# Performance work log

Hardware: AMD Instinct MI355X
Metric: run time of the kernel (lower is better)

## Reference

```python
import jax, jax.numpy as jnp
import numpy as np

B, T, C = 2, 1024, 2048
E, TOPK = 8, 2
F_MOE = 1408
F_SHARED = 5632


def setup_inputs() -> dict:
    key = jax.random.key(0)
    ks = jax.random.split(key, 9)
    s = 0.02
    return {
        "x": jax.random.normal(ks[0], (B, T, C), dtype=jnp.float32),
        "gate_w": jax.random.normal(ks[1], (E, C), dtype=jnp.float32) * s,
        "expert_fc1": jax.random.normal(ks[2], (E, F_MOE, C), dtype=jnp.float32) * s,
        "expert_fc2": jax.random.normal(ks[3], (E, F_MOE, C), dtype=jnp.float32) * s,
        "expert_proj": jax.random.normal(ks[4], (E, C, F_MOE), dtype=jnp.float32) * s,
        "shared_fc1": jax.random.normal(ks[5], (F_SHARED, C), dtype=jnp.float32) * s,
        "shared_fc2": jax.random.normal(ks[6], (F_SHARED, C), dtype=jnp.float32) * s,
        "shared_proj": jax.random.normal(ks[7], (C, F_SHARED), dtype=jnp.float32) * s,
        "shared_gate_w": jax.random.normal(ks[8], (1, C), dtype=jnp.float32) * s,
    }


def reference(x, gate_w, expert_fc1, expert_fc2, expert_proj,
              shared_fc1, shared_fc2, shared_proj, shared_gate_w):
    b, t, c = x.shape
    xf = x.reshape(-1, c)                                   # [N, C]
    n = xf.shape[0]

    # router: softmax in fp32, then top-k
    router = xf @ gate_w.T                                  # [N, E]
    probs = jax.nn.softmax(router.astype(jnp.float32), axis=1).astype(x.dtype)
    top_p, top_i = jax.lax.top_k(probs, TOPK)               # [N, k]

    # dense combine weights: prob where selected else 0 (top-k indices are distinct)
    combine = jnp.zeros((n, E), dtype=x.dtype).at[
        jnp.arange(n)[:, None], top_i].set(top_p)            # [N, E]

    # per-expert SwiGLU MLP, computed densely then weighted by combine
    h1 = jnp.einsum('nc,efc->enf', xf, expert_fc1)          # [E, N, F]
    h2 = jnp.einsum('nc,efc->enf', xf, expert_fc2)
    h = jax.nn.silu(h1) * h2
    out_e = jnp.einsum('enf,ecf->enc', h, expert_proj)      # [E, N, C]
    y = jnp.einsum('ne,enc->nc', combine, out_e)            # [N, C]

    # shared expert with sigmoid gate
    s1 = xf @ shared_fc1.T
    s2 = xf @ shared_fc2.T
    shared = (jax.nn.silu(s1) * s2) @ shared_proj.T         # [N, C]
    y = y + jax.nn.sigmoid(xf @ shared_gate_w.T) * shared
    return y.reshape(b, t, c)
```

## Files before the change

### kernel.cpp

```cpp
#include <hip/hip_runtime.h>
#include <hip/hip_bf16.h>
#include <math.h>
#include <stdint.h>

#define N_TOK   2048
#define C_DIM   2048
#define E_NUM   8
#define F_MOE   1408
#define F_SH    5632
#define SLOTS   4096
#define PADROWS 4608

typedef __bf16 bf16;
typedef __bf16 bf16x8 __attribute__((ext_vector_type(8)));
typedef __bf16 bf16x4 __attribute__((ext_vector_type(4)));
typedef float  f32x4  __attribute__((ext_vector_type(4)));

__device__ __forceinline__ f32x4 mfma16(bf16x8 a, bf16x8 b, f32x4 c) {
    return __builtin_amdgcn_mfma_f32_16x16x32_bf16(a, b, c, 0, 0, 0);
}
__device__ __forceinline__ void gload16(const void* g, void* l) {
    __builtin_amdgcn_global_load_lds(
        (const __attribute__((address_space(1))) void*)g,
        (__attribute__((address_space(3))) void*)l, 16, 0, 0);
}
#define RAWBAR() asm volatile("s_barrier" ::: "memory")
#define VMCNT8() asm volatile("s_waitcnt vmcnt(8)" ::: "memory")
#define VMCNT4() asm volatile("s_waitcnt vmcnt(4)" ::: "memory")
#define VMCNT0() asm volatile("s_waitcnt vmcnt(0)" ::: "memory")

__global__ void router_kernel(const float* __restrict__ x,
                              const float* __restrict__ gate_w,
                              const float* __restrict__ sgate_w,
                              int* __restrict__ slotexp,
                              float* __restrict__ slotp,
                              float* __restrict__ sig)
{
    const int n   = blockIdx.x;
    const int tid = threadIdx.x;
    const float* xr = x + (size_t)n * C_DIM;
    const int c0 = tid * 8;

    float xv[8];
#pragma unroll
    for (int j = 0; j < 8; ++j) xv[j] = xr[c0 + j];

    float dots[9];
#pragma unroll
    for (int e = 0; e < 9; ++e) {
        const float* wr = (e < 8) ? (gate_w + (size_t)e * C_DIM) : sgate_w;
        float p = 0.f;
#pragma unroll
        for (int j = 0; j < 8; ++j) p += xv[j] * wr[c0 + j];
#pragma unroll
        for (int off = 32; off > 0; off >>= 1) p += __shfl_down(p, off);
        dots[e] = p;
    }

    __shared__ float red[4][9];
    const int wid = tid >> 6, lane = tid & 63;
    if (lane == 0) {
#pragma unroll
        for (int e = 0; e < 9; ++e) red[wid][e] = dots[e];
    }
    __syncthreads();
    if (tid == 0) {
        float l[9];
#pragma unroll
        for (int e = 0; e < 9; ++e)
            l[e] = red[0][e] + red[1][e] + red[2][e] + red[3][e];
        float mx = l[0];
#pragma unroll
        for (int e = 1; e < 8; ++e) mx = fmaxf(mx, l[e]);
        float p[8], s = 0.f;
#pragma unroll
        for (int e = 0; e < 8; ++e) { p[e] = expf(l[e] - mx); s += p[e]; }
        const float inv = 1.f / s;
#pragma unroll
        for (int e = 0; e < 8; ++e) p[e] *= inv;
        int i1 = 0;
#pragma unroll
        for (int e = 1; e < 8; ++e) if (p[e] > p[i1]) i1 = e;
        int i2 = (i1 == 0) ? 1 : 0;
#pragma unroll
        for (int e = 0; e < 8; ++e) if (e != i1 && p[e] > p[i2]) i2 = e;
        slotexp[2 * n]     = i1;  slotp[2 * n]     = p[i1];
        slotexp[2 * n + 1] = i2;  slotp[2 * n + 1] = p[i2];
        sig[n] = 1.f / (1.f + expf(-l[8]));
    }
}

__global__ void scatter_kernel(const int* __restrict__ slotexp,
                               int* __restrict__ counts, int* __restrict__ bases,
                               int* __restrict__ pos_of, int* __restrict__ row_token)
{
    const int tid = threadIdx.x;
    const int w = tid >> 6, lane = tid & 63;
    __shared__ int cnt[E_NUM], base[E_NUM];

    int run = 0;
    for (int s0 = 0; s0 < SLOTS; s0 += 64) {
        int e = slotexp[s0 + lane];
        unsigned long long m = __ballot(e == w);
        run += __popcll(m);
    }
    if (lane == 0) cnt[w] = run;
    __syncthreads();
    if (tid == 0) {
        int b = 0;
        for (int e = 0; e < E_NUM; ++e) { base[e] = b; b += cnt[e]; }
    }
    __syncthreads();
    run = 0;
    for (int s0 = 0; s0 < SLOTS; s0 += 64) {
        const int s = s0 + lane;
        const int e = slotexp[s];
        unsigned long long m = __ballot(e == w);
        if (e == w) {
            const unsigned long long lt = (lane == 0) ? 0ull : (~0ull >> (64 - lane));
            const int pos = base[w] + run + __popcll(m & lt);
            pos_of[s]      = pos;
            row_token[pos] = s >> 1;
        }
        run += __popcll(m);
    }
    if (lane == 0) { counts[w] = cnt[w]; bases[w] = base[w]; }
}

struct CvtArgs {
    const float* in[7];
    bf16*        out[7];
    int          cum[8];
};

__global__ void cvt_all_kernel(CvtArgs a)
{
    int b = blockIdx.x;
    int s = 0;
#pragma unroll
    for (int k = 1; k < 7; ++k) s += (b >= a.cum[k]);
    const size_t base = (size_t)(b - a.cum[s]) * 8192;
    const float* in = a.in[s];
    bf16* out = a.out[s];
    const int t4 = threadIdx.x * 4;
    f32x4 v[8];
#pragma unroll
    for (int c = 0; c < 8; ++c)
        v[c] = *(const f32x4*)(in + base + c * 1024 + t4);
#pragma unroll
    for (int c = 0; c < 8; ++c) {
        bf16x4 o;
#pragma unroll
        for (int j = 0; j < 4; ++j) o[j] = (bf16)v[c][j];
        *(bf16x4*)(out + base + c * 1024 + t4) = o;
    }
}

__global__ void gather_kernel(const bf16* __restrict__ Xs,
                              const int* __restrict__ row_token,
                              bf16* __restrict__ Xg)
{
    const int pos = blockIdx.x;
    const int t   = row_token[pos];
    const bf16x8* s = (const bf16x8*)(Xs + (size_t)t * C_DIM);
    bf16x8*       d = (bf16x8*)(Xg + (size_t)pos * C_DIM);
    d[threadIdx.x] = s[threadIdx.x];
}

template<bool DUAL, int KSPLIT>
__device__ __forceinline__ void gemm_body(
    const bf16* __restrict__ A, int lda,
    const bf16* __restrict__ B1g, const bf16* __restrict__ B2g, size_t strideB,
    bf16* __restrict__ OUTh, bf16* __restrict__ OUTq, int ldo, size_t strideOut,
    int base, int cnt, int e, int yt, int nt, int kp, int K, char* lds)
{
    const int KT = (K / 64) / KSPLIT;
    const int H  = 2 * KT;

    const int m0 = base + yt * 256;
    const int tid = threadIdx.x;
    const int w = tid >> 6, lane = tid & 63;

    const int l3  = lane >> 3;
    const int chS = (lane & 7) ^ l3;
    const int hiS = chS >> 2, ccS = chS & 3;
    const int rl  = w * 16 + 2 * l3 + hiS;
    const size_t lda2 = (size_t)lda * 2, K2 = (size_t)K * 2;
    const size_t kpoff = (size_t)kp * KT * 128;

    const char* aSrc0 = (const char*)A + (size_t)(m0 + rl)       * lda2 + ccS * 16 + kpoff;
    const char* aSrc1 = (const char*)A + (size_t)(m0 + 128 + rl) * lda2 + ccS * 16 + kpoff;
    const bf16* B1 = B1g + (size_t)e * strideB;
    const char* bSrc0;
    const char* bSrc1;
    if constexpr (DUAL) {
        const bf16* B2 = B2g + (size_t)e * strideB;
        bSrc0 = (const char*)B1 + (size_t)(nt * 128 + rl) * K2 + ccS * 16 + kpoff;
        bSrc1 = (const char*)B2 + (size_t)(nt * 128 + rl) * K2 + ccS * 16 + kpoff;
    } else {
        bSrc0 = (const char*)B1 + (size_t)(nt * 256 + rl)       * K2 + ccS * 16 + kpoff;
        bSrc1 = (const char*)B1 + (size_t)(nt * 256 + 128 + rl) * K2 + ccS * 16 + kpoff;
    }
    char* ldsw = lds + w * 1024;

    auto issue = [&](int h) {
        const size_t ko = (size_t)(h >> 1) * 128 + (size_t)(h & 1) * 64;
        char* d = ldsw + (h & 3) * 32768;
        gload16(aSrc0 + ko, d);
        gload16(aSrc1 + ko, d + 8192);
        gload16(bSrc0 + ko, d + 16384);
        gload16(bSrc1 + ko, d + 24576);
    };

    const int wm = w >> 2, wn = w & 3;
    const int fr = lane & 15, fq = lane >> 4;
    const int chRd = (((fr & 1) << 2) | fq) ^ ((fr >> 1) & 7);
    uint32_t aOff[8], bOff[4];
#pragma unroll
    for (int m = 0; m < 8; ++m)
        aOff[m] = (uint32_t)((wm * 64 + m * 8 + (fr >> 1)) * 128 + chRd * 16);
#pragma unroll
    for (int n = 0; n < 4; ++n) {
        int rp;
        if constexpr (DUAL)
            rp = (n < 2) ? (wn * 16 + n * 8) : (64 + wn * 16 + (n - 2) * 8);
        else
            rp = wn * 32 + n * 8;
        rp += (fr >> 1);
        bOff[n] = (uint32_t)(16384 + rp * 128 + chRd * 16);
    }

    f32x4 acc[8][4] = {};

    auto compute_half = [&](int h) {
        const char* LB = lds + (h & 3) * 32768;
        bf16x8 af[4], bf[4];
#pragma unroll
        for (int n = 0; n < 4; ++n) bf[n] = *(const bf16x8*)(LB + bOff[n]);
#pragma unroll
        for (int m = 0; m < 4; ++m) af[m] = *(const bf16x8*)(LB + aOff[m]);
        RAWBAR(); __builtin_amdgcn_sched_barrier(0);
        __builtin_amdgcn_s_setprio(1);
#pragma unroll
        for (int m = 0; m < 4; ++m)
#pragma unroll
            for (int n = 0; n < 4; ++n)
                acc[m][n] = mfma16(af[m], bf[n], acc[m][n]);
        __builtin_amdgcn_s_setprio(0);
#pragma unroll
        for (int m = 0; m < 4; ++m) af[m] = *(const bf16x8*)(LB + aOff[4 + m]);
        RAWBAR(); __builtin_amdgcn_sched_barrier(0);
        __builtin_amdgcn_s_setprio(1);
#pragma unroll
        for (int m = 0; m < 4; ++m)
#pragma unroll
            for (int n = 0; n < 4; ++n)
                acc[4 + m][n] = mfma16(af[m], bf[n], acc[4 + m][n]);
        __builtin_amdgcn_s_setprio(0);
    };

    issue(0); issue(1); issue(2);

    for (int h = 0; h < H - 3; ++h) {
        VMCNT8();
        RAWBAR();
        issue(h + 3);
        compute_half(h);
    }
    VMCNT8(); RAWBAR(); compute_half(H - 3);
    VMCNT4(); RAWBAR(); compute_half(H - 2);
    VMCNT0(); RAWBAR(); compute_half(H - 1);

    const int rb0 = m0 + wm * 128;
    const int rend = base + cnt;
#pragma unroll
    for (int m = 0; m < 8; ++m) {
#pragma unroll
        for (int j = 0; j < 4; ++j) {
            const int grow = rb0 + m * 16 + fq * 4 + j;
            if (grow >= rend) continue;
            if constexpr (DUAL) {
#pragma unroll
                for (int n = 0; n < 2; ++n) {
                    const int gcol = nt * 128 + wn * 32 + n * 16 + fr;
                    const float h1 = acc[m][n][j];
                    const float h2 = acc[m][n + 2][j];
                    OUTh[(size_t)grow * ldo + gcol] =
                        (bf16)(h1 / (1.f + expf(-h1)) * h2);
                }
            } else {
                bf16* O = OUTq + (size_t)kp * strideOut;
#pragma unroll
                for (int n = 0; n < 4; ++n) {
                    const int gcol = nt * 256 + wn * 64 + n * 16 + fr;
                    O[(size_t)grow * ldo + gcol] = (bf16)acc[m][n][j];
                }
            }
        }
    }
}

template<bool DUAL, bool GROUPED, int KSPLIT>
__global__ __launch_bounds__(512, 1)
void gemm8(const bf16* __restrict__ A, int lda,
           const bf16* __restrict__ B1g, const bf16* __restrict__ B2g,
           size_t strideB,
           bf16* __restrict__ OUTh, bf16* __restrict__ OUTq, int ldo,
           size_t strideOut,
           const int* __restrict__ bases, const int* __restrict__ counts,
           int K)
{
    __shared__ char lds[131072];
    int e, yt, nt, kp, base, cnt;
    if constexpr (GROUPED) {
        e = blockIdx.x; yt = blockIdx.y; nt = blockIdx.z; kp = 0;
        base = bases[e]; cnt = counts[e];
        if (yt * 256 >= cnt) return;
    } else {
        nt = blockIdx.x; yt = blockIdx.y; kp = (KSPLIT > 1) ? blockIdx.z : 0;
        e = 0; base = 0; cnt = N_TOK;
    }
    gemm_body<DUAL, KSPLIT>(A, lda, B1g, B2g, strideB, OUTh, OUTq, ldo,
                            strideOut, base, cnt, e, yt, nt, kp, K, lds);
}

#define FC0_TILES 352

__global__ __launch_bounds__(512, 1)
void gemm_fc(const bf16* __restrict__ Xs, const bf16* __restrict__ Xg,
             const bf16* __restrict__ Wsfc1, const bf16* __restrict__ Wsfc2,
             const bf16* __restrict__ Wefc1, const bf16* __restrict__ Wefc2,
             bf16* __restrict__ Hs, bf16* __restrict__ Hm,
             const int* __restrict__ bases, const int* __restrict__ counts)
{
    __shared__ char lds[131072];
    const int id = blockIdx.x;
    if (id < FC0_TILES) {
        const int nt = id % 44, yt = id / 44;
        gemm_body<true, 1>(Xs, C_DIM, Wsfc1, Wsfc2, 0, Hs, nullptr, F_SH, 0,
                           0, N_TOK, 0, yt, nt, 0, C_DIM, lds);
    } else {
        const int lid = id - FC0_TILES;
        const int e = lid & 7, yt = (lid >> 3) & 15, nt = lid >> 7;
        const int base = bases[e], cnt = counts[e];
        if (yt * 256 >= cnt) return;
        gemm_body<true, 1>(Xg, C_DIM, Wefc1, Wefc2, (size_t)F_MOE * C_DIM,
                           Hm, nullptr, F_MOE, 0,
                           base, cnt, e, yt, nt, 0, C_DIM, lds);
    }
}

__global__ void combine_kernel(const bf16* __restrict__ SP,
                               const bf16* __restrict__ EP,
                               const int* __restrict__ pos_of,
                               const float* __restrict__ slotp,
                               const float* __restrict__ sig,
                               float* __restrict__ y)
{
    const int n  = blockIdx.x;
    const int p0 = pos_of[2 * n], p1 = pos_of[2 * n + 1];
    const float w0 = slotp[2 * n], w1 = slotp[2 * n + 1], sg = sig[n];
    const size_t PS = (size_t)N_TOK * C_DIM;
    const size_t cidx = (size_t)n * C_DIM + threadIdx.x * 8;

    bf16x8 s0 = *(const bf16x8*)(SP + cidx);
    bf16x8 s1 = *(const bf16x8*)(SP + cidx + PS);
    bf16x8 s2 = *(const bf16x8*)(SP + cidx + 2 * PS);
    bf16x8 s3 = *(const bf16x8*)(SP + cidx + 3 * PS);
    bf16x8 a0 = *(const bf16x8*)(EP + (size_t)p0 * C_DIM + threadIdx.x * 8);
    bf16x8 a1 = *(const bf16x8*)(EP + (size_t)p1 * C_DIM + threadIdx.x * 8);

    float out[8];
#pragma unroll
    for (int j = 0; j < 8; ++j) {
        const float ssum = (float)s0[j] + (float)s1[j] + (float)s2[j] + (float)s3[j];
        out[j] = sg * ssum + w0 * (float)a0[j] + w1 * (float)a1[j];
    }
    f32x4 o0, o1;
#pragma unroll
    for (int j = 0; j < 4; ++j) { o0[j] = out[j]; o1[j] = out[4 + j]; }
    *(f32x4*)(y + cidx)     = o0;
    *(f32x4*)(y + cidx + 4) = o1;
}

extern "C" void kernel_launch(void* const* d_in, const int* in_sizes, int n_in,
                              void* d_out, int out_size, void* d_ws, size_t ws_size,
                              hipStream_t stream)
{
    const float* x     = (const float*)d_in[0];
    const float* gatew = (const float*)d_in[1];
    const float* efc1  = (const float*)d_in[2];
    const float* efc2  = (const float*)d_in[3];
    const float* eproj = (const float*)d_in[4];
    const float* sfc1  = (const float*)d_in[5];
    const float* sfc2  = (const float*)d_in[6];
    const float* sproj = (const float*)d_in[7];
    const float* sgate = (const float*)d_in[8];
    float* y = (float*)d_out;

    char* w = (char*)d_ws;
    size_t off = 0;
    auto take = [&](size_t bytes) {
        char* p = w + off;
        off = (off + bytes + 255) & ~(size_t)255;
        return p;
    };
    int*   counts    = (int*)  take(E_NUM * 4);
    int*   bases     = (int*)  take(E_NUM * 4);
    int*   slotexp   = (int*)  take(SLOTS * 4);
    float* slotp     = (float*)take(SLOTS * 4);
    int*   pos_of    = (int*)  take(SLOTS * 4);
    int*   row_token = (int*)  take(PADROWS * 4);
    float* sig       = (float*)take(N_TOK * 4);
    bf16*  Xs        = (bf16*) take((size_t)N_TOK   * C_DIM * 2);
    bf16*  Xg        = (bf16*) take((size_t)PADROWS * C_DIM * 2);
    bf16*  Hs        = (bf16*) take((size_t)N_TOK   * F_SH  * 2);
    bf16*  Hm        = (bf16*) take((size_t)PADROWS * F_MOE * 2);
    bf16*  SP        = (bf16*) take((size_t)4 * N_TOK * C_DIM * 2);
    bf16*  EP        = (bf16*) take((size_t)PADROWS * C_DIM * 2);
    bf16*  Wefc1     = (bf16*) take((size_t)E_NUM * F_MOE * C_DIM * 2);
    bf16*  Wefc2     = (bf16*) take((size_t)E_NUM * F_MOE * C_DIM * 2);
    bf16*  Weproj    = (bf16*) take((size_t)E_NUM * C_DIM * F_MOE * 2);
    bf16*  Wsfc1     = (bf16*) take((size_t)F_SH * C_DIM * 2);
    bf16*  Wsfc2     = (bf16*) take((size_t)F_SH * C_DIM * 2);
    bf16*  Wsproj    = (bf16*) take((size_t)C_DIM * F_SH * 2);
    (void)ws_size; (void)in_sizes; (void)n_in; (void)out_size;

    CvtArgs ca;
    const int nbx  = (N_TOK * C_DIM) / 8192;
    const int nbe  = (E_NUM * F_MOE * C_DIM) / 8192;
    const int nbs  = (F_SH * C_DIM) / 8192;
    ca.in[0] = x;     ca.out[0] = Xs;
    ca.in[1] = efc1;  ca.out[1] = Wefc1;
    ca.in[2] = efc2;  ca.out[2] = Wefc2;
    ca.in[3] = eproj; ca.out[3] = Weproj;
    ca.in[4] = sfc1;  ca.out[4] = Wsfc1;
    ca.in[5] = sfc2;  ca.out[5] = Wsfc2;
    ca.in[6] = sproj; ca.out[6] = Wsproj;
    ca.cum[0] = 0;
    ca.cum[1] = nbx;
    ca.cum[2] = nbx + nbe;
    ca.cum[3] = nbx + 2 * nbe;
    ca.cum[4] = nbx + 3 * nbe;
    ca.cum[5] = nbx + 3 * nbe + nbs;
    ca.cum[6] = nbx + 3 * nbe + 2 * nbs;
    ca.cum[7] = nbx + 3 * nbe + 3 * nbs;
    cvt_all_kernel<<<ca.cum[7], 256, 0, stream>>>(ca);

    router_kernel<<<N_TOK, 256, 0, stream>>>(x, gatew, sgate, slotexp, slotp, sig);
    scatter_kernel<<<1, 512, 0, stream>>>(slotexp, counts, bases, pos_of, row_token);
    gather_kernel<<<SLOTS, 256, 0, stream>>>(Xs, row_token, Xg);

    gemm_fc<<<FC0_TILES + E_NUM * (SLOTS / 256) * (F_MOE / 128), 512, 0, stream>>>(
        Xs, Xg, Wsfc1, Wsfc2, Wefc1, Wefc2, Hs, Hm, bases, counts);

    gemm8<false, false, 4><<<dim3(C_DIM / 256, N_TOK / 256, 4), 512, 0, stream>>>(
        Hs, F_SH, Wsproj, nullptr, 0, nullptr, SP, C_DIM, (size_t)N_TOK * C_DIM,
        nullptr, nullptr, F_SH);

    gemm8<false, true, 1><<<dim3(E_NUM, SLOTS / 256, C_DIM / 256), 512, 0, stream>>>(
        Hm, F_MOE, Weproj, nullptr, (size_t)C_DIM * F_MOE, nullptr, EP, C_DIM, 0,
        bases, counts, F_MOE);

    combine_kernel<<<N_TOK, 256, 0, stream>>>(SP, EP, pos_of, slotp, sig, y);
}
```

Measured before the change: 448.1 us.

## Fuse fp32-to-bf16 weight conversion into GEMM B-tile loading

Drops the standalone pass that converted all expert and shared weights to bf16. The GEMMs now read fp32 weights directly into registers, convert them, and write bf16 into LDS, while the A operand keeps the async global-to-LDS path. The pipeline is rebuilt with two register buffers, adjusted vmcnt waits and an lgkm wait before each barrier. This removes a full read-and-write of every weight, but doubles the weight bytes each GEMM tile fetches and, since tiles re-read weights, repeats the conversion work. The extra VGPR pressure and VALU conversion sit in the inner loop.

Measured after the change: 473.1 us. +5.6%, slower.

```diff
diff --git a/kernel.cpp b/kernel.cpp
--- a/kernel.cpp
+++ b/kernel.cpp
@@ -26,8 +26,10 @@
 }
 #define RAWBAR() asm volatile("s_barrier" ::: "memory")
 #define VMCNT8() asm volatile("s_waitcnt vmcnt(8)" ::: "memory")
-#define VMCNT4() asm volatile("s_waitcnt vmcnt(4)" ::: "memory")
+#define VMCNT6() asm volatile("s_waitcnt vmcnt(6)" ::: "memory")
 #define VMCNT0() asm volatile("s_waitcnt vmcnt(0)" ::: "memory")
+#define LGKM0()  asm volatile("s_waitcnt lgkmcnt(0)" ::: "memory")
+#define CFENCE() asm volatile("" ::: "memory")
 
 __global__ void router_kernel(const float* __restrict__ x,
                               const float* __restrict__ gate_w,
@@ -127,21 +129,9 @@
     if (lane == 0) { counts[w] = cnt[w]; bases[w] = base[w]; }
 }
 
-struct CvtArgs {
-    const float* in[7];
-    bf16*        out[7];
-    int          cum[8];
-};
-
-__global__ void cvt_all_kernel(CvtArgs a)
-{
-    int b = blockIdx.x;
-    int s = 0;
-#pragma unroll
-    for (int k = 1; k < 7; ++k) s += (b >= a.cum[k]);
-    const size_t base = (size_t)(b - a.cum[s]) * 8192;
-    const float* in = a.in[s];
-    bf16* out = a.out[s];
+__global__ void cvt_x_kernel(const float* __restrict__ in, bf16* __restrict__ out)
+{
+    const size_t base = (size_t)blockIdx.x * 8192;
     const int t4 = threadIdx.x * 4;
     f32x4 v[8];
 #pragma unroll
@@ -170,7 +160,7 @@
 template<bool DUAL, int KSPLIT>
 __device__ __forceinline__ void gemm_body(
     const bf16* __restrict__ A, int lda,
-    const bf16* __restrict__ B1g, const bf16* __restrict__ B2g, size_t strideB,
+    const float* __restrict__ B1g, const float* __restrict__ B2g, size_t strideB,
     bf16* __restrict__ OUTh, bf16* __restrict__ OUTq, int ldo, size_t strideOut,
     int base, int cnt, int e, int yt, int nt, int kp, int K, char* lds)
 {
@@ -185,31 +175,49 @@
     const int chS = (lane & 7) ^ l3;
     const int hiS = chS >> 2, ccS = chS & 3;
     const int rl  = w * 16 + 2 * l3 + hiS;
-    const size_t lda2 = (size_t)lda * 2, K2 = (size_t)K * 2;
-    const size_t kpoff = (size_t)kp * KT * 128;
-
-    const char* aSrc0 = (const char*)A + (size_t)(m0 + rl)       * lda2 + ccS * 16 + kpoff;
-    const char* aSrc1 = (const char*)A + (size_t)(m0 + 128 + rl) * lda2 + ccS * 16 + kpoff;
-    const bf16* B1 = B1g + (size_t)e * strideB;
-    const char* bSrc0;
-    const char* bSrc1;
+    const size_t lda2 = (size_t)lda * 2;
+    const size_t K4 = (size_t)K * 4;
+    const size_t kpoffA = (size_t)kp * KT * 128;
+    const size_t kpoffB = (size_t)kp * KT * 256;
+
+    const char* aSrc0 = (const char*)A + (size_t)(m0 + rl)       * lda2 + ccS * 16 + kpoffA;
+    const char* aSrc1 = (const char*)A + (size_t)(m0 + 128 + rl) * lda2 + ccS * 16 + kpoffA;
+    const float* B1 = B1g + (size_t)e * strideB;
+    const char* bSrc0f;
+    const char* bSrc1f;
     if constexpr (DUAL) {
-        const bf16* B2 = B2g + (size_t)e * strideB;
-        bSrc0 = (const char*)B1 + (size_t)(nt * 128 + rl) * K2 + ccS * 16 + kpoff;
-        bSrc1 = (const char*)B2 + (size_t)(nt * 128 + rl) * K2 + ccS * 16 + kpoff;
+        const float* B2 = B2g + (size_t)e * strideB;
+        bSrc0f = (const char*)B1 + (size_t)(nt * 128 + rl) * K4 + ccS * 32 + kpoffB;
+        bSrc1f = (const char*)B2 + (size_t)(nt * 128 + rl) * K4 + ccS * 32 + kpoffB;
     } else {
-        bSrc0 = (const char*)B1 + (size_t)(nt * 256 + rl)       * K2 + ccS * 16 + kpoff;
-        bSrc1 = (const char*)B1 + (size_t)(nt * 256 + 128 + rl) * K2 + ccS * 16 + kpoff;
+        bSrc0f = (const char*)B1 + (size_t)(nt * 256 + rl)       * K4 + ccS * 32 + kpoffB;
+        bSrc1f = (const char*)B1 + (size_t)(nt * 256 + 128 + rl) * K4 + ccS * 32 + kpoffB;
     }
     char* ldsw = lds + w * 1024;
 
-    auto issue = [&](int h) {
+    auto issueA = [&](int h) {
         const size_t ko = (size_t)(h >> 1) * 128 + (size_t)(h & 1) * 64;
         char* d = ldsw + (h & 3) * 32768;
         gload16(aSrc0 + ko, d);
         gload16(aSrc1 + ko, d + 8192);
-        gload16(bSrc0 + ko, d + 16384);
-        gload16(bSrc1 + ko, d + 24576);
+    };
+    auto issueB = [&](int h, f32x4 (&set)[4]) {
+        const size_t ko = (size_t)(h >> 1) * 256 + (size_t)(h & 1) * 128;
+        set[0] = *(const f32x4*)(bSrc0f + ko);
+        set[1] = *(const f32x4*)(bSrc0f + ko + 16);
+        set[2] = *(const f32x4*)(bSrc1f + ko);
+        set[3] = *(const f32x4*)(bSrc1f + ko + 16);
+    };
+    auto writeB = [&](int h, f32x4 (&set)[4]) {
+        bf16x8 w0, w1;
+#pragma unroll
+        for (int j = 0; j < 4; ++j) {
+            w0[j] = (bf16)set[0][j]; w0[4 + j] = (bf16)set[1][j];
+            w1[j] = (bf16)set[2][j]; w1[4 + j] = (bf16)set[3][j];
+        }
+        char* bd = ldsw + (h & 3) * 32768 + 16384 + lane * 16;
+        *(bf16x8*)bd = w0;
+        *(bf16x8*)(bd + 8192) = w1;
     };
 
     const int wm = w >> 2, wn = w & 3;
@@ -259,17 +267,30 @@
         __builtin_amdgcn_s_setprio(0);
     };
 
-    issue(0); issue(1); issue(2);
-
-    for (int h = 0; h < H - 3; ++h) {
-        VMCNT8();
+    f32x4 bsA[4], bsB[4];
+
+    auto ITER = [&](int h, f32x4 (&set)[4], int wc) {
+        if (wc == 8) { VMCNT8(); } else if (wc == 6) { VMCNT6(); } else { VMCNT0(); }
+        writeB(h, set);
+        LGKM0();
         RAWBAR();
-        issue(h + 3);
+        if (h + 2 < H) { issueB(h + 2, set); } CFENCE();
+        if (h + 3 < H) { issueA(h + 3); }    CFENCE();
         compute_half(h);
-    }
-    VMCNT8(); RAWBAR(); compute_half(H - 3);
-    VMCNT4(); RAWBAR(); compute_half(H - 2);
-    VMCNT0(); RAWBAR(); compute_half(H - 1);
+    };
+
+    issueA(0); CFENCE();
+    issueB(0, bsA); CFENCE();
+    issueA(1); CFENCE();
+    issueB(1, bsB); CFENCE();
+    issueA(2); CFENCE();
+
+    for (int h = 0; h < H - 2; h += 2) {
+        ITER(h, bsA, 8);
+        ITER(h + 1, bsB, 8);
+    }
+    ITER(H - 2, bsA, 6);
+    ITER(H - 1, bsB, 0);
 
     const int rb0 = m0 + wm * 128;
     const int rend = base + cnt;
@@ -303,7 +324,7 @@
 template<bool DUAL, bool GROUPED, int KSPLIT>
 __global__ __launch_bounds__(512, 1)
 void gemm8(const bf16* __restrict__ A, int lda,
-           const bf16* __restrict__ B1g, const bf16* __restrict__ B2g,
+           const float* __restrict__ B1g, const float* __restrict__ B2g,
            size_t strideB,
            bf16* __restrict__ OUTh, bf16* __restrict__ OUTq, int ldo,
            size_t strideOut,
@@ -328,8 +349,8 @@
 
 __global__ __launch_bounds__(512, 1)
 void gemm_fc(const bf16* __restrict__ Xs, const bf16* __restrict__ Xg,
-             const bf16* __restrict__ Wsfc1, const bf16* __restrict__ Wsfc2,
-             const bf16* __restrict__ Wefc1, const bf16* __restrict__ Wefc2,
+             const float* __restrict__ sfc1, const float* __restrict__ sfc2,
+             const float* __restrict__ efc1, const float* __restrict__ efc2,
              bf16* __restrict__ Hs, bf16* __restrict__ Hm,
              const int* __restrict__ bases, const int* __restrict__ counts)
 {
@@ -337,14 +358,14 @@
     const int id = blockIdx.x;
     if (id < FC0_TILES) {
         const int nt = id % 44, yt = id / 44;
-        gemm_body<true, 1>(Xs, C_DIM, Wsfc1, Wsfc2, 0, Hs, nullptr, F_SH, 0,
+        gemm_body<true, 1>(Xs, C_DIM, sfc1, sfc2, 0, Hs, nullptr, F_SH, 0,
                            0, N_TOK, 0, yt, nt, 0, C_DIM, lds);
     } else {
         const int lid = id - FC0_TILES;
         const int e = lid & 7, yt = (lid >> 3) & 15, nt = lid >> 7;
         const int base = bases[e], cnt = counts[e];
         if (yt * 256 >= cnt) return;
-        gemm_body<true, 1>(Xg, C_DIM, Wefc1, Wefc2, (size_t)F_MOE * C_DIM,
+        gemm_body<true, 1>(Xg, C_DIM, efc1, efc2, (size_t)F_MOE * C_DIM,
                            Hm, nullptr, F_MOE, 0,
                            base, cnt, e, yt, nt, 0, C_DIM, lds);
     }
@@ -418,48 +439,23 @@
     bf16*  Hm        = (bf16*) take((size_t)PADROWS * F_MOE * 2);
     bf16*  SP        = (bf16*) take((size_t)4 * N_TOK * C_DIM * 2);
     bf16*  EP        = (bf16*) take((size_t)PADROWS * C_DIM * 2);
-    bf16*  Wefc1     = (bf16*) take((size_t)E_NUM * F_MOE * C_DIM * 2);
-    bf16*  Wefc2     = (bf16*) take((size_t)E_NUM * F_MOE * C_DIM * 2);
-    bf16*  Weproj    = (bf16*) take((size_t)E_NUM * C_DIM * F_MOE * 2);
-    bf16*  Wsfc1     = (bf16*) take((size_t)F_SH * C_DIM * 2);
-    bf16*  Wsfc2     = (bf16*) take((size_t)F_SH * C_DIM * 2);
-    bf16*  Wsproj    = (bf16*) take((size_t)C_DIM * F_SH * 2);
     (void)ws_size; (void)in_sizes; (void)n_in; (void)out_size;
 
-    CvtArgs ca;
-    const int nbx  = (N_TOK * C_DIM) / 8192;
-    const int nbe  = (E_NUM * F_MOE * C_DIM) / 8192;
-    const int nbs  = (F_SH * C_DIM) / 8192;
-    ca.in[0] = x;     ca.out[0] = Xs;
-    ca.in[1] = efc1;  ca.out[1] = Wefc1;
-    ca.in[2] = efc2;  ca.out[2] = Wefc2;
-    ca.in[3] = eproj; ca.out[3] = Weproj;
-    ca.in[4] = sfc1;  ca.out[4] = Wsfc1;
-    ca.in[5] = sfc2;  ca.out[5] = Wsfc2;
-    ca.in[6] = sproj; ca.out[6] = Wsproj;
-    ca.cum[0] = 0;
-    ca.cum[1] = nbx;
-    ca.cum[2] = nbx + nbe;
-    ca.cum[3] = nbx + 2 * nbe;
-    ca.cum[4] = nbx + 3 * nbe;
-    ca.cum[5] = nbx + 3 * nbe + nbs;
-    ca.cum[6] = nbx + 3 * nbe + 2 * nbs;
-    ca.cum[7] = nbx + 3 * nbe + 3 * nbs;
-    cvt_all_kernel<<<ca.cum[7], 256, 0, stream>>>(ca);
+    cvt_x_kernel<<<(N_TOK * C_DIM) / 8192, 256, 0, stream>>>(x, Xs);
 
     router_kernel<<<N_TOK, 256, 0, stream>>>(x, gatew, sgate, slotexp, slotp, sig);
     scatter_kernel<<<1, 512, 0, stream>>>(slotexp, counts, bases, pos_of, row_token);
     gather_kernel<<<SLOTS, 256, 0, stream>>>(Xs, row_token, Xg);
 
     gemm_fc<<<FC0_TILES + E_NUM * (SLOTS / 256) * (F_MOE / 128), 512, 0, stream>>>(
-        Xs, Xg, Wsfc1, Wsfc2, Wefc1, Wefc2, Hs, Hm, bases, counts);
+        Xs, Xg, sfc1, sfc2, efc1, efc2, Hs, Hm, bases, counts);
 
     gemm8<false, false, 4><<<dim3(C_DIM / 256, N_TOK / 256, 4), 512, 0, stream>>>(
-        Hs, F_SH, Wsproj, nullptr, 0, nullptr, SP, C_DIM, (size_t)N_TOK * C_DIM,
+        Hs, F_SH, sproj, nullptr, 0, nullptr, SP, C_DIM, (size_t)N_TOK * C_DIM,
         nullptr, nullptr, F_SH);
 
     gemm8<false, true, 1><<<dim3(E_NUM, SLOTS / 256, C_DIM / 256), 512, 0, stream>>>(
-        Hm, F_MOE, Weproj, nullptr, (size_t)C_DIM * F_MOE, nullptr, EP, C_DIM, 0,
+        Hm, F_MOE, eproj, nullptr, (size_t)C_DIM * F_MOE, nullptr, EP, C_DIM, 0,
         bases, counts, F_MOE);
 
     combine_kernel<<<N_TOK, 256, 0, stream>>>(SP, EP, pos_of, slotp, sig, y);
```
